# Performance work log

Hardware: AMD Instinct MI355X
Metric: run time of the kernel (lower is better)

Reference implementation:

```python
import jax, jax.numpy as jnp
import numpy as np

B, T, E, U, V = 4096, 80, 100, 64, 10000

def setup_inputs() -> dict:
    key = jax.random.key(0)
    ks = jax.random.split(key, 10)
    s = lambda *sh: 0.05
    return {
        "tokens": jax.random.randint(ks[0], (B, T), 0, V, dtype=jnp.int32),
        "emb": jax.random.normal(ks[1], (V, E), jnp.float32) * 0.05,
        "k0": jax.random.normal(ks[2], (E, 4 * U), jnp.float32) * 0.05,
        "r0": jax.random.normal(ks[3], (U, 4 * U), jnp.float32) * 0.05,
        "b0": jnp.zeros((4 * U,), jnp.float32),
        "k1": jax.random.normal(ks[4], (E, 4 * U), jnp.float32) * 0.05,
        "r1": jax.random.normal(ks[5], (U, 4 * U), jnp.float32) * 0.05,
        "b1": jnp.zeros((4 * U,), jnp.float32),
        "Wd": jax.random.normal(ks[6], (U, 1), jnp.float32) * 0.05,
        "bd": jnp.zeros((1,), jnp.float32),
    }

def _lstm_cell(h, c, xt, k, r, b):
    # keras LSTMCell gate order: i, f, g(cell candidate), o
    z = xt @ k + h @ r + b  # [B, 4U]
    i, f, g, o = jnp.split(z, 4, axis=-1)
    c_new = jax.nn.sigmoid(f) * c + jax.nn.sigmoid(i) * jnp.tanh(g)
    h_new = jax.nn.sigmoid(o) * jnp.tanh(c_new)
    return h_new, c_new

def reference(tokens, emb, k0, r0, b0, k1, r1, b1, Wd, bd):
    x = emb[tokens]                 # [B, T, E]
    xs = jnp.swapaxes(x, 0, 1)      # [T, B, E] for scan over time
    zeros = jnp.zeros((tokens.shape[0], U), x.dtype)
    init = (zeros, zeros, zeros, zeros)  # h0, c0, h1, c1

    def step(state, xt):
        h0, c0, h1, c1 = state
        h0, c0 = _lstm_cell(h0, c0, xt, k0, r0, b0)
        # NOTE: original feeds the raw embedded word (not out0) to cell 1
        h1, c1 = _lstm_cell(h1, c1, xt, k1, r1, b1)
        return (h0, c0, h1, c1), None

    (h0, c0, h1, c1), _ = jax.lax.scan(step, init, xs)
    logits = h1 @ Wd + bd           # [B, 1]
    return jax.nn.sigmoid(logits)
```

## Files before the change

kernel.cpp:

```cpp
#include <hip/hip_runtime.h>
#include <hip/hip_bf16.h>

#define B_  4096
#define T_  80
#define E_  100
#define U_  64
#define G_  256
#define V_  10000

#define S_H  72

typedef __attribute__((ext_vector_type(8))) __bf16 bf16x8;
typedef __attribute__((ext_vector_type(4))) __bf16 bf16x4;
typedef __attribute__((ext_vector_type(4))) float  floatx4;

__device__ __forceinline__ float sigmoidf_(float x) {
    return __fdividef(1.f, 1.f + __expf(-x));
}

__device__ __forceinline__ float tanhf_(float x) {
    return 1.f - __fdividef(2.f, __expf(2.f * x) + 1.f);
}

__device__ __forceinline__ void lds_barrier_() {
    asm volatile("s_waitcnt lgkmcnt(0)\n\ts_barrier" ::: "memory");
}

__global__ __launch_bounds__(256) void embk_kernel(const float* __restrict__ emb,
                                                   const float* __restrict__ k1,
                                                   const float* __restrict__ b1,
                                                   float* __restrict__ embk) {
    const int tid  = threadIdx.x;
    const int lane = tid & 63;
    const int w    = tid >> 6;
    const int n    = lane & 15;
    const int kg   = lane >> 4;
    const int v0   = (blockIdx.x >> 1) * 16;
    const int n0   = (blockIdx.x & 1) * 128;

    const float* erow = emb + (long)(v0 + n) * E_ + kg * 8;
    bf16x8 afr[4];
#pragma unroll
    for (int kc = 0; kc < 3; ++kc) {
        float4 e0 = *(const float4*)(erow + kc * 32);
        float4 e1 = *(const float4*)(erow + kc * 32 + 4);
        bf16x8 s;
        s[0] = (__bf16)e0.x; s[1] = (__bf16)e0.y; s[2] = (__bf16)e0.z; s[3] = (__bf16)e0.w;
        s[4] = (__bf16)e1.x; s[5] = (__bf16)e1.y; s[6] = (__bf16)e1.z; s[7] = (__bf16)e1.w;
        afr[kc] = s;
    }
    {
        bf16x8 s;
#pragma unroll
        for (int jj = 0; jj < 8; ++jj) s[jj] = (__bf16)0.f;
        if (kg == 0) {
            float4 e0 = *(const float4*)(erow + 96);
            s[0] = (__bf16)e0.x; s[1] = (__bf16)e0.y; s[2] = (__bf16)e0.z; s[3] = (__bf16)e0.w;
        }
        afr[3] = s;
    }

    bf16x8 bfr[2][4];
#pragma unroll
    for (int ct = 0; ct < 2; ++ct)
#pragma unroll
        for (int kc = 0; kc < 4; ++kc) {
            bf16x8 s;
#pragma unroll
            for (int jj = 0; jj < 8; ++jj) {
                int k = kc * 32 + kg * 8 + jj;
                s[jj] = (k < E_) ? (__bf16)k1[k * G_ + n0 + w * 32 + ct * 16 + n]
                                 : (__bf16)0.f;
            }
            bfr[ct][kc] = s;
        }

#pragma unroll
    for (int ct = 0; ct < 2; ++ct) {
        float bv = b1[n0 + w * 32 + ct * 16 + n];
        floatx4 acc = {bv, bv, bv, bv};
        acc = __builtin_amdgcn_mfma_f32_16x16x32_bf16(afr[0], bfr[ct][0], acc, 0, 0, 0);
        acc = __builtin_amdgcn_mfma_f32_16x16x32_bf16(afr[1], bfr[ct][1], acc, 0, 0, 0);
        acc = __builtin_amdgcn_mfma_f32_16x16x32_bf16(afr[2], bfr[ct][2], acc, 0, 0, 0);
        acc = __builtin_amdgcn_mfma_f32_16x16x32_bf16(afr[3], bfr[ct][3], acc, 0, 0, 0);
#pragma unroll
        for (int r = 0; r < 4; ++r)
            embk[(long)(v0 + kg * 4 + r) * G_ + n0 + w * 32 + ct * 16 + n] = acc[r];
    }
}

__global__ __launch_bounds__(256) void lstm_kernel(const int*   __restrict__ tokens,
                                                   const float* __restrict__ embk,
                                                   const float* __restrict__ r1,
                                                   const float* __restrict__ Wd,
                                                   const float* __restrict__ bd,
                                                   float* __restrict__ out) {
    __shared__ int    tokLDS[16 * T_];
    __shared__ __bf16 hbuf[2][16 * S_H];

    const int tid  = threadIdx.x;
    const int lane = tid & 63;
    const int w    = tid >> 6;
    const int n    = lane & 15;
    const int kg   = lane >> 4;
    const int bb   = blockIdx.x * 16;

    for (int i = tid; i < 16 * T_; i += 256) tokLDS[i] = tokens[bb * T_ + i];
    for (int i = tid; i < 2 * 16 * S_H; i += 256) (&hbuf[0][0])[i] = (__bf16)0.f;

    bf16x8 afr[4][2];
#pragma unroll
    for (int ct = 0; ct < 4; ++ct)
#pragma unroll
        for (int kc = 0; kc < 2; ++kc) {
            bf16x8 s;
#pragma unroll
            for (int jj = 0; jj < 8; ++jj)
                s[jj] = (__bf16)r1[(kc * 32 + kg * 8 + jj) * G_ + ct * 64 + w * 16 + n];
            afr[ct][kc] = s;
        }

    float c[4] = {0.f, 0.f, 0.f, 0.f};

    __syncthreads();

    floatx4 xkb[2][4];
#pragma unroll
    for (int s = 0; s < 2; ++s) {
        const float* base = embk + (long)tokLDS[n * T_ + s] * G_ + w * 16 + kg * 4;
#pragma unroll
        for (int ct = 0; ct < 4; ++ct)
            xkb[s][ct] = *(const floatx4*)(base + ct * 64);
    }

    auto step = [&](int t, int sel) {
        const __bf16* hb = hbuf[sel ^ 1];
        bf16x8 b0 = *(const bf16x8*)(hb + n * S_H + kg * 8);
        bf16x8 b1 = *(const bf16x8*)(hb + n * S_H + 32 + kg * 8);

        floatx4 acc[4];
#pragma unroll
        for (int ct = 0; ct < 4; ++ct) {
            floatx4 a = xkb[sel][ct];
            a = __builtin_amdgcn_mfma_f32_16x16x32_bf16(afr[ct][0], b0, a, 0, 0, 0);
            a = __builtin_amdgcn_mfma_f32_16x16x32_bf16(afr[ct][1], b1, a, 0, 0, 0);
            acc[ct] = a;
        }

        if (t + 2 < T_) {
            const float* base = embk + (long)tokLDS[n * T_ + t + 2] * G_ + w * 16 + kg * 4;
#pragma unroll
            for (int ct = 0; ct < 4; ++ct)
                xkb[sel][ct] = *(const floatx4*)(base + ct * 64);
        }

        bf16x4 hv;
#pragma unroll
        for (int r = 0; r < 4; ++r) {
            float zi = acc[0][r], zf = acc[1][r], zg = acc[2][r], zo = acc[3][r];
            float cn = sigmoidf_(zf) * c[r] + sigmoidf_(zi) * tanhf_(zg);
            float hn = sigmoidf_(zo) * tanhf_(cn);
            c[r] = cn;
            hv[r] = (__bf16)hn;
        }
        *(bf16x4*)(&hbuf[sel][0] + n * S_H + w * 16 + kg * 4) = hv;

        lds_barrier_();
    };

    for (int t = 0; t < T_; t += 2) {
        step(t,     0);
        step(t + 1, 1);
    }

    if (tid < 16) {
        const __bf16* hb = hbuf[1] + tid * S_H;
        float s = bd[0];
#pragma unroll
        for (int u = 0; u < U_; ++u) s = fmaf((float)hb[u], Wd[u], s);
        out[bb + tid] = sigmoidf_(s);
    }
}

extern "C" void kernel_launch(void* const* d_in, const int* in_sizes, int n_in,
                              void* d_out, int out_size, void* d_ws, size_t ws_size,
                              hipStream_t stream) {
    const int*   tokens = (const int*)  d_in[0];
    const float* emb    = (const float*)d_in[1];
    const float* k1     = (const float*)d_in[5];
    const float* r1     = (const float*)d_in[6];
    const float* b1     = (const float*)d_in[7];
    const float* Wd     = (const float*)d_in[8];
    const float* bd     = (const float*)d_in[9];
    float*       out    = (float*)d_out;

    float* embk = (float*)d_ws;

    embk_kernel<<<(V_ / 16) * 2, 256, 0, stream>>>(emb, k1, b1, embk);
    lstm_kernel<<<B_ / 16, 256, 0, stream>>>(tokens, embk, r1, Wd, bd, out);
}
```

Baseline: 161.1 us.

## Compute input projection inside LSTM loop from bf16 embeddings instead of precomputed table

```diff
diff --git a/kernel.cpp b/kernel.cpp
--- a/kernel.cpp
+++ b/kernel.cpp
@@ -9,6 +9,8 @@
 #define V_  10000
 
 #define S_H  72
+#define TP   81
+#define EK   128
 
 typedef __attribute__((ext_vector_type(8))) __bf16 bf16x8;
 typedef __attribute__((ext_vector_type(4))) __bf16 bf16x4;
@@ -26,76 +28,24 @@
     asm volatile("s_waitcnt lgkmcnt(0)\n\ts_barrier" ::: "memory");
 }
 
-__global__ __launch_bounds__(256) void embk_kernel(const float* __restrict__ emb,
-                                                   const float* __restrict__ k1,
-                                                   const float* __restrict__ b1,
-                                                   float* __restrict__ embk) {
-    const int tid  = threadIdx.x;
-    const int lane = tid & 63;
-    const int w    = tid >> 6;
-    const int n    = lane & 15;
-    const int kg   = lane >> 4;
-    const int v0   = (blockIdx.x >> 1) * 16;
-    const int n0   = (blockIdx.x & 1) * 128;
-
-    const float* erow = emb + (long)(v0 + n) * E_ + kg * 8;
-    bf16x8 afr[4];
-#pragma unroll
-    for (int kc = 0; kc < 3; ++kc) {
-        float4 e0 = *(const float4*)(erow + kc * 32);
-        float4 e1 = *(const float4*)(erow + kc * 32 + 4);
-        bf16x8 s;
-        s[0] = (__bf16)e0.x; s[1] = (__bf16)e0.y; s[2] = (__bf16)e0.z; s[3] = (__bf16)e0.w;
-        s[4] = (__bf16)e1.x; s[5] = (__bf16)e1.y; s[6] = (__bf16)e1.z; s[7] = (__bf16)e1.w;
-        afr[kc] = s;
-    }
-    {
-        bf16x8 s;
-#pragma unroll
-        for (int jj = 0; jj < 8; ++jj) s[jj] = (__bf16)0.f;
-        if (kg == 0) {
-            float4 e0 = *(const float4*)(erow + 96);
-            s[0] = (__bf16)e0.x; s[1] = (__bf16)e0.y; s[2] = (__bf16)e0.z; s[3] = (__bf16)e0.w;
-        }
-        afr[3] = s;
-    }
-
-    bf16x8 bfr[2][4];
-#pragma unroll
-    for (int ct = 0; ct < 2; ++ct)
-#pragma unroll
-        for (int kc = 0; kc < 4; ++kc) {
-            bf16x8 s;
-#pragma unroll
-            for (int jj = 0; jj < 8; ++jj) {
-                int k = kc * 32 + kg * 8 + jj;
-                s[jj] = (k < E_) ? (__bf16)k1[k * G_ + n0 + w * 32 + ct * 16 + n]
-                                 : (__bf16)0.f;
-            }
-            bfr[ct][kc] = s;
-        }
-
-#pragma unroll
-    for (int ct = 0; ct < 2; ++ct) {
-        float bv = b1[n0 + w * 32 + ct * 16 + n];
-        floatx4 acc = {bv, bv, bv, bv};
-        acc = __builtin_amdgcn_mfma_f32_16x16x32_bf16(afr[0], bfr[ct][0], acc, 0, 0, 0);
-        acc = __builtin_amdgcn_mfma_f32_16x16x32_bf16(afr[1], bfr[ct][1], acc, 0, 0, 0);
-        acc = __builtin_amdgcn_mfma_f32_16x16x32_bf16(afr[2], bfr[ct][2], acc, 0, 0, 0);
-        acc = __builtin_amdgcn_mfma_f32_16x16x32_bf16(afr[3], bfr[ct][3], acc, 0, 0, 0);
-#pragma unroll
-        for (int r = 0; r < 4; ++r)
-            embk[(long)(v0 + kg * 4 + r) * G_ + n0 + w * 32 + ct * 16 + n] = acc[r];
-    }
+__global__ __launch_bounds__(256) void embbf_kernel(const float* __restrict__ emb,
+                                                    __bf16* __restrict__ embbf) {
+    const int idx = blockIdx.x * 256 + threadIdx.x;
+    const int v   = idx >> 7;
+    const int col = idx & (EK - 1);
+    float x = (col < E_) ? emb[(long)v * E_ + col] : 0.f;
+    embbf[idx] = (__bf16)x;
 }
 
-__global__ __launch_bounds__(256) void lstm_kernel(const int*   __restrict__ tokens,
-                                                   const float* __restrict__ embk,
-                                                   const float* __restrict__ r1,
-                                                   const float* __restrict__ Wd,
-                                                   const float* __restrict__ bd,
-                                                   float* __restrict__ out) {
-    __shared__ int    tokLDS[16 * T_];
+__global__ __launch_bounds__(256, 1) void lstm_kernel(const int*   __restrict__ tokens,
+                                                      const __bf16* __restrict__ embbf,
+                                                      const float* __restrict__ k1,
+                                                      const float* __restrict__ r1,
+                                                      const float* __restrict__ b1,
+                                                      const float* __restrict__ Wd,
+                                                      const float* __restrict__ bd,
+                                                      float* __restrict__ out) {
+    __shared__ int    tokLDS[16 * TP];
     __shared__ __bf16 hbuf[2][16 * S_H];
 
     const int tid  = threadIdx.x;
@@ -105,8 +55,26 @@
     const int kg   = lane >> 4;
     const int bb   = blockIdx.x * 16;
 
-    for (int i = tid; i < 16 * T_; i += 256) tokLDS[i] = tokens[bb * T_ + i];
+    for (int i = tid; i < 16 * T_; i += 256) {
+        int r = i / T_, t = i - r * T_;
+        tokLDS[r * TP + t] = tokens[bb * T_ + i];
+    }
     for (int i = tid; i < 2 * 16 * S_H; i += 256) (&hbuf[0][0])[i] = (__bf16)0.f;
+
+    bf16x8 akr[4][4];
+#pragma unroll
+    for (int ct = 0; ct < 4; ++ct)
+#pragma unroll
+        for (int kc = 0; kc < 4; ++kc) {
+            bf16x8 s;
+#pragma unroll
+            for (int jj = 0; jj < 8; ++jj) {
+                int k = kc * 32 + kg * 8 + jj;
+                s[jj] = (k < E_) ? (__bf16)k1[k * G_ + ct * 64 + w * 16 + n]
+                                 : (__bf16)0.f;
+            }
+            akr[ct][kc] = s;
+        }
 
     bf16x8 afr[4][2];
 #pragma unroll
@@ -120,38 +88,49 @@
             afr[ct][kc] = s;
         }
 
+    floatx4 bias[4];
+#pragma unroll
+    for (int ct = 0; ct < 4; ++ct)
+#pragma unroll
+        for (int r = 0; r < 4; ++r)
+            bias[ct][r] = b1[ct * 64 + w * 16 + kg * 4 + r];
+
     float c[4] = {0.f, 0.f, 0.f, 0.f};
 
     __syncthreads();
 
-    floatx4 xkb[2][4];
+    bf16x8 xe[2][4];
 #pragma unroll
     for (int s = 0; s < 2; ++s) {
-        const float* base = embk + (long)tokLDS[n * T_ + s] * G_ + w * 16 + kg * 4;
+        const __bf16* base = embbf + (long)tokLDS[n * TP + s] * EK + kg * 8;
 #pragma unroll
-        for (int ct = 0; ct < 4; ++ct)
-            xkb[s][ct] = *(const floatx4*)(base + ct * 64);
+        for (int kc = 0; kc < 4; ++kc)
+            xe[s][kc] = *(const bf16x8*)(base + kc * 32);
     }
 
     auto step = [&](int t, int sel) {
         const __bf16* hb = hbuf[sel ^ 1];
         bf16x8 b0 = *(const bf16x8*)(hb + n * S_H + kg * 8);
-        bf16x8 b1 = *(const bf16x8*)(hb + n * S_H + 32 + kg * 8);
+        bf16x8 b1v = *(const bf16x8*)(hb + n * S_H + 32 + kg * 8);
 
         floatx4 acc[4];
 #pragma unroll
         for (int ct = 0; ct < 4; ++ct) {
-            floatx4 a = xkb[sel][ct];
-            a = __builtin_amdgcn_mfma_f32_16x16x32_bf16(afr[ct][0], b0, a, 0, 0, 0);
-            a = __builtin_amdgcn_mfma_f32_16x16x32_bf16(afr[ct][1], b1, a, 0, 0, 0);
+            floatx4 a = bias[ct];
+            a = __builtin_amdgcn_mfma_f32_16x16x32_bf16(akr[ct][0], xe[sel][0], a, 0, 0, 0);
+            a = __builtin_amdgcn_mfma_f32_16x16x32_bf16(akr[ct][1], xe[sel][1], a, 0, 0, 0);
+            a = __builtin_amdgcn_mfma_f32_16x16x32_bf16(akr[ct][2], xe[sel][2], a, 0, 0, 0);
+            a = __builtin_amdgcn_mfma_f32_16x16x32_bf16(akr[ct][3], xe[sel][3], a, 0, 0, 0);
+            a = __builtin_amdgcn_mfma_f32_16x16x32_bf16(afr[ct][0], b0,  a, 0, 0, 0);
+            a = __builtin_amdgcn_mfma_f32_16x16x32_bf16(afr[ct][1], b1v, a, 0, 0, 0);
             acc[ct] = a;
         }
 
         if (t + 2 < T_) {
-            const float* base = embk + (long)tokLDS[n * T_ + t + 2] * G_ + w * 16 + kg * 4;
+            const __bf16* base = embbf + (long)tokLDS[n * TP + t + 2] * EK + kg * 8;
 #pragma unroll
-            for (int ct = 0; ct < 4; ++ct)
-                xkb[sel][ct] = *(const floatx4*)(base + ct * 64);
+            for (int kc = 0; kc < 4; ++kc)
+                xe[sel][kc] = *(const bf16x8*)(base + kc * 32);
         }
 
         bf16x4 hv;
@@ -194,8 +173,8 @@
     const float* bd     = (const float*)d_in[9];
     float*       out    = (float*)d_out;
 
-    float* embk = (float*)d_ws;
+    __bf16* embbf = (__bf16*)d_ws;
 
-    embk_kernel<<<(V_ / 16) * 2, 256, 0, stream>>>(emb, k1, b1, embk);
-    lstm_kernel<<<B_ / 16, 256, 0, stream>>>(tokens, embk, r1, Wd, bd, out);
+    embbf_kernel<<<V_ * EK / 256, 256, 0, stream>>>(emb, embbf);
+    lstm_kernel<<<B_ / 16, 256, 0, stream>>>(tokens, embbf, k1, r1, b1, Wd, bd, out);
 }
```

After: 161.0 us. No clear change (-0.1%).
